# Optimization experiments

Hardware: AMD Instinct MI355X
Metric: run time of the kernel (lower is better)

The kernel has to match this reference:

```python
import jax, jax.numpy as jnp
import numpy as np
import math

N = 4096      # nodes
E = 131072    # edges
D = 256       # hidden / out_features
DIN = 16      # distance_map feature dim
H = 2         # attention heads
HD = D // H   # head dim = 128


def setup_inputs() -> dict:
    key = jax.random.key(0)
    ks = jax.random.split(key, 20)
    s = 0.02
    return {
        "input": jax.random.normal(ks[0], (N, D), jnp.float32),
        "adj": jax.random.randint(ks[1], (2, E), 0, N, jnp.int64),
        "h0": jax.random.normal(ks[2], (N, D), jnp.float32),
        "lamda": 1,
        "alpha": jax.random.uniform(ks[3], (1,), jnp.float32),
        "l": 1,
        "distance_map": jax.random.normal(ks[4], (E, DIN), jnp.float32),
        "norm": jax.random.uniform(ks[5], (E,), jnp.float32),
        # GraphConvolution params
        "weight_local": jax.random.normal(ks[6], (2 * D, D), jnp.float32) * s,
        "weight_global": jax.random.normal(ks[7], (2 * D, D), jnp.float32) * s,
        # EA_GCN.lin : Linear(16, D)
        "lin_w": jax.random.normal(ks[8], (D, DIN), jnp.float32) * s,
        "lin_b": jnp.zeros((D,), jnp.float32),
        # EA_GCN.W_EV : 3D -> 2D -> D -> 16 (GELU between)
        "w1": jax.random.normal(ks[9], (2 * D, 3 * D), jnp.float32) * s,
        "b1": jnp.zeros((2 * D,), jnp.float32),
        "w2": jax.random.normal(ks[10], (D, 2 * D), jnp.float32) * s,
        "b2": jnp.zeros((D,), jnp.float32),
        "w3": jax.random.normal(ks[11], (DIN, D), jnp.float32) * s,
        "b3": jnp.zeros((DIN,), jnp.float32),
        # MultiheadAttention params (torch layout: in_proj [3D, D])
        "in_proj_w": jax.random.normal(ks[12], (3 * D, D), jnp.float32) * s,
        "in_proj_b": jnp.zeros((3 * D,), jnp.float32),
        "out_proj_w": jax.random.normal(ks[13], (D, D), jnp.float32) * s,
        "out_proj_b": jnp.zeros((D,), jnp.float32),
    }


def _mha(x, wi, bi, wo, bo):
    # torch MHA, unbatched (N, D) input, eval mode (dropout off)
    qkv = x @ wi.T + bi                      # [N, 3D]
    q, k, v = jnp.split(qkv, 3, axis=-1)
    q = q.reshape(N, H, HD).transpose(1, 0, 2)  # [H, N, HD]
    k = k.reshape(N, H, HD).transpose(1, 0, 2)
    v = v.reshape(N, H, HD).transpose(1, 0, 2)
    scores = jnp.einsum("hnd,hmd->hnm", q, k) / math.sqrt(HD)
    attn = jax.nn.softmax(scores, axis=-1)
    o = jnp.einsum("hnm,hmd->hnd", attn, v)     # [H, N, HD]
    o = o.transpose(1, 0, 2).reshape(N, D)
    return o @ wo.T + bo


def _ea_gcn(x, edge_index, norm, distance_map, lin_w, lin_b, w1, b1, w2, b2, w3, b3):
    src, dst = edge_index[0], edge_index[1]
    edge_attr = distance_map @ lin_w.T + lin_b               # [E, D]
    msg = norm[:, None] * (x[src] + edge_attr)               # gather + combine
    agg = jax.ops.segment_sum(msg, dst, num_segments=N)      # scatter-add
    x_out = agg + x
    h = jnp.concatenate([x_out[src], edge_attr, x_out[dst]], axis=-1)  # [E, 3D]
    h = jax.nn.gelu(h @ w1.T + b1, approximate=False)
    h = jax.nn.gelu(h @ w2.T + b2, approximate=False)
    dm_out = h @ w3.T + b3                                   # [E, 16]
    return x_out, dm_out


def reference(input, adj, h0, lamda, alpha, l, distance_map, norm,
              weight_local, weight_global, lin_w, lin_b,
              w1, b1, w2, b2, w3, b3,
              in_proj_w, in_proj_b, out_proj_w, out_proj_b):
    theta = min(1.0, math.log(lamda / l + 1.0))
    a = alpha[0]
    h_local, dm_out = _ea_gcn(input, adj, norm, distance_map,
                              lin_w, lin_b, w1, b1, w2, b2, w3, b3)
    h_global = _mha(input, in_proj_w, in_proj_b, out_proj_w, out_proj_b)
    support_local = jnp.concatenate([h_local, h0], axis=1)   # [N, 2D]
    r_local = (1.0 - a) * h_local + a * h0
    support_global = jnp.concatenate([h_global, h0], axis=1)
    r_global = (1.0 - a) * h_global + a * h0
    output_local = theta * (support_local @ weight_local) + (1.0 - theta) * r_local
    output_global = theta * (support_global @ weight_global) + (1.0 - theta) * r_global
    output = output_local + output_global                    # residual=False
    return (output, dm_out)
```

## Files before the change

### kernel.cpp

```cpp
#include <hip/hip_runtime.h>
#include <hip/hip_bf16.h>
#include <math.h>

constexpr int N_   = 4096;
constexpr int E_   = 131072;
constexpr int D_   = 256;
constexpr int DIN_ = 16;
constexpr int D3_  = 768;
constexpr int HD_  = 128;

typedef __bf16 bf16_8 __attribute__((ext_vector_type(8)));
typedef float  f32x4  __attribute__((ext_vector_type(4)));
typedef float  f32x4v __attribute__((ext_vector_type(4)));
typedef unsigned int u32x4 __attribute__((ext_vector_type(4)));

__device__ __forceinline__ unsigned short f2b(float f) {
  unsigned int u = __float_as_uint(f);
  u = u + 0x7fffu + ((u >> 16) & 1u);
  return (unsigned short)(u >> 16);
}
__device__ __forceinline__ float b2f(unsigned short s) {
  return __uint_as_float(((unsigned int)s) << 16);
}
__device__ __forceinline__ unsigned int pack2(unsigned short lo, unsigned short hi) {
  return (unsigned int)lo | ((unsigned int)hi << 16);
}
__device__ __forceinline__ bf16_8 frag16(const unsigned short* p) {
  uint4 v = *(const uint4*)p;
  return __builtin_bit_cast(bf16_8, v);
}
__device__ __forceinline__ float4 ntload4(const void* p) {
  f32x4v v = __builtin_nontemporal_load((const f32x4v*)p);
  float4 r;
  r.x = v[0]; r.y = v[1]; r.z = v[2]; r.w = v[3];
  return r;
}
__device__ __forceinline__ void ntstore16(void* dst, uint4 v) {
  __builtin_nontemporal_store(__builtin_bit_cast(u32x4, v), (u32x4*)dst);
}
__device__ __forceinline__ void gl2lds16(const unsigned short* g, unsigned short* l) {
  __builtin_amdgcn_global_load_lds(
      (const __attribute__((address_space(1))) void*)g,
      (__attribute__((address_space(3))) void*)l, 16, 0, 0);
}

__device__ __forceinline__ float scalar_as_float(const void* p) {
  int iv = *(const int*)p;
  if (iv >= 1 && iv <= 1000000) return (float)iv;
  return __int_as_float(iv);
}

__device__ __forceinline__ float gelu_exact(float v) {
  return 0.5f * v * (1.0f + erff(v * 0.70710678118654752f));
}
__device__ __forceinline__ float gelu_fast(float v) {
  float u = 0.7978845608028654f * v * (1.0f + 0.044715f * v * v);
  return v / (1.0f + __expf(-2.0f * u));
}

__global__ void k_f2b(const float* __restrict__ src, unsigned short* __restrict__ dst, int n) {
  int i = blockIdx.x * 256 + threadIdx.x;
  if (i < n) dst[i] = f2b(src[i]);
}

__global__ void k_prep_w(const float* __restrict__ w1, const float* __restrict__ w2,
                         const float* __restrict__ w3, const float* __restrict__ lin_w,
                         const float* __restrict__ ipw, const float* __restrict__ opw,
                         unsigned short* __restrict__ wb1, unsigned short* __restrict__ wb2,
                         unsigned short* __restrict__ wb3, unsigned short* __restrict__ lwb,
                         unsigned short* __restrict__ wqb, unsigned short* __restrict__ opwb) {
  int i = blockIdx.x * 256 + threadIdx.x;
  if (i < 393216) { wb1[i] = f2b(w1[i]); return; }
  i -= 393216;
  if (i < 131072) { wb2[i] = f2b(w2[i]); return; }
  i -= 131072;
  if (i < 4096) { wb3[i] = f2b(w3[i]); return; }
  i -= 4096;
  if (i < 4096) { lwb[i] = f2b(lin_w[i]); return; }
  i -= 4096;
  if (i < 196608) { wqb[i] = f2b(ipw[i]); return; }
  i -= 196608;
  if (i < 65536) { opwb[i] = f2b(opw[i]); }
}

__global__ void k_prep_t(const float* __restrict__ Wl, const float* __restrict__ Wg,
                         unsigned short* __restrict__ wlT, unsigned short* __restrict__ wgT) {
  int i = blockIdx.x * 256 + threadIdx.x;
  int seg = i >> 17;
  int idx = i & 131071;
  int k = idx & 511, j = idx >> 9;
  const float* src = seg ? Wg : Wl;
  unsigned short* dst = seg ? wgT : wlT;
  dst[idx] = f2b(src[(size_t)k * 256 + j]);
}

__global__ void k_prep_x(const float* __restrict__ input, const float* __restrict__ h0,
                         unsigned short* __restrict__ inb, unsigned short* __restrict__ h0b) {
  int i = blockIdx.x * 256 + threadIdx.x;
  int seg = i >> 20;
  int idx = i & 1048575;
  if (seg) h0b[idx] = f2b(h0[idx]);
  else     inb[idx] = f2b(input[idx]);
}

__global__ void k_copy4(const float4* __restrict__ src, float4* __restrict__ dst, int n4) {
  int idx = blockIdx.x * 256 + threadIdx.x;
  if (idx < n4) dst[idx] = src[idx];
}

__global__ __launch_bounds__(256) void k_edge_attr_mfma(
    const float* __restrict__ dmap, const unsigned short* __restrict__ lwb,
    const float* __restrict__ lin_b, unsigned short* __restrict__ eab) {
  __shared__ unsigned short sT[4][16][264];
  const int tid  = threadIdx.x;
  const int lane = tid & 63, wv = tid >> 6;
  const int r16  = lane & 15, quad = lane >> 4;
  const int e0   = blockIdx.x * 64 + wv * 16;

  const uint4 z4 = make_uint4(0u, 0u, 0u, 0u);
  bf16_8 bfr[16];
#pragma unroll
  for (int n = 0; n < 16; ++n) {
    uint4 v = z4;
    if (quad < 2) v = *(const uint4*)(lwb + (size_t)(n * 16 + r16) * DIN_ + quad * 8);
    bfr[n] = __builtin_bit_cast(bf16_8, v);
  }
  bf16_8 af;
  {
    uint4 p = z4;
    if (quad < 2) {
      const float4* dp = (const float4*)(dmap + (size_t)(e0 + r16) * DIN_ + quad * 8);
      float4 a = dp[0], b = dp[1];
      p = make_uint4(pack2(f2b(a.x), f2b(a.y)), pack2(f2b(a.z), f2b(a.w)),
                     pack2(f2b(b.x), f2b(b.y)), pack2(f2b(b.z), f2b(b.w)));
    }
    af = __builtin_bit_cast(bf16_8, p);
  }

  const f32x4 zz = {0.f, 0.f, 0.f, 0.f};
  f32x4 acc[16];
#pragma unroll
  for (int n = 0; n < 16; ++n) acc[n] = zz;
#pragma unroll
  for (int n = 0; n < 16; ++n)
    acc[n] = __builtin_amdgcn_mfma_f32_16x16x32_bf16(af, bfr[n], acc[n], 0, 0, 0);

#pragma unroll
  for (int n = 0; n < 16; ++n) {
    float bb = lin_b[n * 16 + r16];
#pragma unroll
    for (int rg = 0; rg < 4; ++rg)
      sT[wv][quad * 4 + rg][n * 16 + r16] = f2b(acc[n][rg] + bb);
  }
#pragma unroll
  for (int it = 0; it < 8; ++it) {
    int flat = it * 64 + lane;
    int row = flat >> 5, g = flat & 31;
    uint4 v = *(const uint4*)&sT[wv][row][g * 8];
    ntstore16(&eab[(size_t)(e0 + row) * D_ + g * 8], v);
  }
}

__global__ void k_zero(int* __restrict__ p, int n) {
  int i = blockIdx.x * 256 + threadIdx.x;
  if (i < n) p[i] = 0;
}
__global__ void k_hist(const int* __restrict__ adj, int* __restrict__ cnt) {
  int e = blockIdx.x * 256 + threadIdx.x;
  atomicAdd(&cnt[adj[E_ + e]], 1);
}
__global__ __launch_bounds__(1024) void k_scan(const int* __restrict__ cnt,
                                               int* __restrict__ off, int* __restrict__ cur) {
  __shared__ int ps[1024];
  int tid = threadIdx.x;
  int base = tid * 4;
  int a0 = cnt[base], a1 = cnt[base + 1], a2 = cnt[base + 2], a3 = cnt[base + 3];
  int tsum = a0 + a1 + a2 + a3;
  ps[tid] = tsum;
  __syncthreads();
  for (int st = 1; st < 1024; st <<= 1) {
    int v = (tid >= st) ? ps[tid - st] : 0;
    __syncthreads();
    ps[tid] += v;
    __syncthreads();
  }
  int excl = ps[tid] - tsum;
  int o0 = excl, o1 = excl + a0, o2 = o1 + a1, o3 = o2 + a2;
  off[base] = o0; off[base + 1] = o1; off[base + 2] = o2; off[base + 3] = o3;
  cur[base] = o0; cur[base + 1] = o1; cur[base + 2] = o2; cur[base + 3] = o3;
  if (tid == 1023) off[4096] = o3 + a3;
}
__global__ void k_bucket(const int* __restrict__ adj, int* __restrict__ cur,
                         int* __restrict__ perm) {
  int e = blockIdx.x * 256 + threadIdx.x;
  int p = atomicAdd(&cur[adj[E_ + e]], 1);
  perm[p] = e;
}
__global__ __launch_bounds__(256) void k_gather(
    const float* __restrict__ x, const int* __restrict__ adj,
    const unsigned short* __restrict__ eab, const float* __restrict__ nrm,
    const int* __restrict__ off, const int* __restrict__ perm,
    float* __restrict__ xout) {
  int n = blockIdx.x, t = threadIdx.x;
  int beg = off[n], end = off[n + 1];
  float acc = x[(size_t)n * D_ + t];
  int i = beg;
  for (; i + 1 < end; i += 2) {
    int e0 = perm[i], e1 = perm[i + 1];
    int s0 = adj[e0], s1 = adj[e1];
    float w0 = nrm[e0], w1 = nrm[e1];
    float xa = x[(size_t)s0 * D_ + t];
    float xb = x[(size_t)s1 * D_ + t];
    float ea0 = b2f(eab[(size_t)e0 * D_ + t]);
    float ea1 = b2f(eab[(size_t)e1 * D_ + t]);
    acc += w0 * (xa + ea0) + w1 * (xb + ea1);
  }
  if (i < end) {
    int e0 = perm[i];
    int s0 = adj[e0];
    float w0 = nrm[e0];
    acc += w0 * (x[(size_t)s0 * D_ + t] + b2f(eab[(size_t)e0 * D_ + t]));
  }
  xout[(size_t)n * D_ + t] = acc;
}

__global__ __launch_bounds__(256) void k_scatter(
    const float* __restrict__ x, const int* __restrict__ adj,
    const float* __restrict__ dmap, const float* __restrict__ nrm,
    const float* __restrict__ lin_w, const float* __restrict__ lin_b,
    float* __restrict__ xout) {
  __shared__ float s_dm[4][DIN_];
  int te = threadIdx.x >> 6;
  int d4 = threadIdx.x & 63;
  int e  = blockIdx.x * 4 + te;
  if (d4 < DIN_) s_dm[te][d4] = dmap[(size_t)e * DIN_ + d4];
  __syncthreads();
  int vs = adj[e];
  int vd = adj[E_ + e];
  float w = nrm[e];
  int d = d4 * 4;
  float4 xs = *(const float4*)(x + (size_t)vs * D_ + d);
  float ea[4];
#pragma unroll
  for (int q = 0; q < 4; q++) {
    const float* lw = lin_w + (size_t)(d + q) * DIN_;
    float acc = lin_b[d + q];
#pragma unroll
    for (int k = 0; k < DIN_; k++) acc += s_dm[te][k] * lw[k];
    ea[q] = acc;
  }
  float* op = xout + (size_t)vd * D_ + d;
  atomicAdd(op + 0, w * (xs.x + ea[0]));
  atomicAdd(op + 1, w * (xs.y + ea[1]));
  atomicAdd(op + 2, w * (xs.z + ea[2]));
  atomicAdd(op + 3, w * (xs.w + ea[3]));
}

__global__ __launch_bounds__(256) void k_gemm_bt(
    const float* __restrict__ A, const float* __restrict__ B,
    const float* __restrict__ bias, float* __restrict__ C,
    int M, int Nn, int K) {
  __shared__ float sA[16][68];
  __shared__ float sB[16][68];
  int bm = blockIdx.y * 64, bn = blockIdx.x * 64;
  int tid = threadIdx.x;
  int tr = tid >> 4, tc = tid & 15;
  float acc[4][4] = {};
  for (int k0 = 0; k0 < K; k0 += 16) {
    for (int i = tid; i < 1024; i += 256) {
      int r = i >> 4, c = i & 15;
      sA[c][r] = A[(size_t)(bm + r) * K + k0 + c];
      sB[c][r] = B[(size_t)(bn + r) * K + k0 + c];
    }
    __syncthreads();
#pragma unroll
    for (int kk = 0; kk < 16; kk++) {
      float av[4], bv[4];
#pragma unroll
      for (int i = 0; i < 4; i++) av[i] = sA[kk][tr * 4 + i];
#pragma unroll
      for (int j = 0; j < 4; j++) bv[j] = sB[kk][tc * 4 + j];
#pragma unroll
      for (int i = 0; i < 4; i++)
#pragma unroll
        for (int j = 0; j < 4; j++) acc[i][j] += av[i] * bv[j];
    }
    __syncthreads();
  }
#pragma unroll
  for (int i = 0; i < 4; i++) {
    int r = bm + tr * 4 + i;
#pragma unroll
    for (int j = 0; j < 4; j++) {
      int c = bn + tc * 4 + j;
      C[(size_t)r * Nn + c] = acc[i][j] + bias[c];
    }
  }
}

__global__ __launch_bounds__(256) void k_qkv_mfma(
    const unsigned short* __restrict__ inb, const unsigned short* __restrict__ wqb,
    const float* __restrict__ ipb, float* __restrict__ qkv) {
  __shared__ unsigned short sA[128][72];
  __shared__ unsigned short sB[128][72];
  const int b   = blockIdx.x;
  const int j0  = (b % 6) * 128;
  const int m0  = (b / 6) * 128;
  const int tid = threadIdx.x;
  const int lane = tid & 63, wv = tid >> 6;
  const int r16  = lane & 15, quad = lane >> 4;
  const int sr   = tid >> 1, sh = (tid & 1) * 32;

  const unsigned short* ra = inb + (size_t)(m0 + sr) * D_;
  const unsigned short* rb = wqb + (size_t)(j0 + sr) * D_;

  const f32x4 zz = {0.f, 0.f, 0.f, 0.f};
  f32x4 acc[2][8];
#pragma unroll
  for (int m = 0; m < 2; ++m)
#pragma unroll
    for (int n = 0; n < 8; ++n) acc[m][n] = zz;

  for (int ki = 0; ki < 4; ++ki) {
    __syncthreads();
    {
      const uint4* s    = (const uint4*)(ra + ki * 64 + sh);
      const uint4* bsrc = (const uint4*)(rb + ki * 64 + sh);
      uint4* da = (uint4*)&sA[sr][sh];
      uint4* db = (uint4*)&sB[sr][sh];
#pragma unroll
      for (int i = 0; i < 4; ++i) { da[i] = s[i]; db[i] = bsrc[i]; }
    }
    __syncthreads();
#pragma unroll
    for (int kk = 0; kk < 2; ++kk) {
      bf16_8 a0 = frag16(&sA[wv * 32 + r16][kk * 32 + quad * 8]);
      bf16_8 a1 = frag16(&sA[wv * 32 + 16 + r16][kk * 32 + quad * 8]);
#pragma unroll
      for (int n = 0; n < 8; ++n) {
        bf16_8 bf = frag16(&sB[n * 16 + r16][kk * 32 + quad * 8]);
        acc[0][n] = __builtin_amdgcn_mfma_f32_16x16x32_bf16(a0, bf, acc[0][n], 0, 0, 0);
        acc[1][n] = __builtin_amdgcn_mfma_f32_16x16x32_bf16(a1, bf, acc[1][n], 0, 0, 0);
      }
    }
  }
#pragma unroll
  for (int m = 0; m < 2; ++m)
#pragma unroll
    for (int n = 0; n < 8; ++n) {
      int col = j0 + n * 16 + r16;
      float bb = ipb[col];
#pragma unroll
      for (int rg = 0; rg < 4; ++rg) {
        int row = m0 + wv * 32 + m * 16 + quad * 4 + rg;
        qkv[(size_t)row * D3_ + col] = acc[m][n][rg] + bb;
      }
    }
}

__global__ __launch_bounds__(256) void k_node_pac(
    const unsigned short* __restrict__ xbp, const unsigned short* __restrict__ wb1,
    unsigned short* __restrict__ Pac) {
  __shared__ unsigned short sA[128][72];
  __shared__ unsigned short sB[128][72];
  const int b    = blockIdx.x;
  const int j0   = (b & 7) * 128;
  const int m0   = (b >> 3) * 128;
  const int side = j0 >> 9;
  const int jr   = j0 - side * 512;
  const int tid  = threadIdx.x;
  const int lane = tid & 63, wv = tid >> 6;
  const int r16  = lane & 15, quad = lane >> 4;
  const int sr   = tid >> 1, sh = (tid & 1) * 32;

  const unsigned short* ra = xbp + (size_t)(m0 + sr) * D_;
  const unsigned short* rb = wb1 + (size_t)(jr + sr) * 768 + side * 512;
// ... 242 lines not shown
  const int lane = tid & 63;
  const int wv   = tid >> 6;
  const int r16  = lane & 15;
  const int quad = lane >> 4;

  bf16_8 qf[4];
#pragma unroll
  for (int kk = 0; kk < 4; ++kk)
    qf[kk] = frag16(Qb + (size_t)h * N_ * HD_ + (size_t)(q0 + r16) * HD_ + kk * 32 + quad * 8);

  if (tid < 16) { sm[tid] = -1e30f; sl[tid] = 0.f; }

  const f32x4 zz = {0.f, 0.f, 0.f, 0.f};
  f32x4 o0 = zz, o1 = zz;

  const unsigned short* Kh = Kb + (size_t)h * N_ * HD_;
  const unsigned short* Vh = Vt + (size_t)h * HD_ * N_;

  for (int c0 = 0; c0 < N_; c0 += 64) {
    __syncthreads();
#pragma unroll
    for (int it = 0; it < 4; ++it) {
      int off = (tid + it * 256) * 8;
      int key = off >> 7, d = off & 127;
      *(uint4*)&sK[key][d] = *(const uint4*)(Kh + (size_t)(c0 + key) * HD_ + d);
    }
#pragma unroll
    for (int it = 0; it < 4; ++it) {
      int off = (tid + it * 256) * 8;
      int d = off >> 6, k = off & 63;
      *(uint4*)&sV[d][k] = *(const uint4*)(Vh + (size_t)d * N_ + c0 + k);
    }
    __syncthreads();
    f32x4 s = zz;
#pragma unroll
    for (int kk = 0; kk < 4; ++kk) {
      bf16_8 bf = frag16(&sK[wv * 16 + r16][kk * 32 + quad * 8]);
      s = __builtin_amdgcn_mfma_f32_16x16x32_bf16(qf[kk], bf, s, 0, 0, 0);
    }
    const float sc = 0.08838834764831845f;
#pragma unroll
    for (int r = 0; r < 4; ++r)
      sS[quad * 4 + r][wv * 16 + r16] = s[r] * sc;
    __syncthreads();
    {
      int row = tid >> 4, i = tid & 15;
      float4 v = *(const float4*)&sS[row][i * 4];
      float mx = fmaxf(fmaxf(v.x, v.y), fmaxf(v.z, v.w));
#pragma unroll
      for (int m = 1; m <= 8; m <<= 1) mx = fmaxf(mx, __shfl_xor(mx, m));
      float mo = sm[row];
      float mn = fmaxf(mo, mx);
      float p0 = __expf(v.x - mn), p1 = __expf(v.y - mn);
      float p2 = __expf(v.z - mn), p3 = __expf(v.w - mn);
      float ps = p0 + p1 + p2 + p3;
#pragma unroll
      for (int m = 1; m <= 8; m <<= 1) ps += __shfl_xor(ps, m);
      uint2 pk = {pack2(f2b(p0), f2b(p1)), pack2(f2b(p2), f2b(p3))};
      *(uint2*)&sP[row][i * 4] = pk;
      if (i == 0) {
        float al = __expf(mo - mn);
        sl[row] = sl[row] * al + ps;
        sm[row] = mn;
        sa[row] = al;
      }
    }
    __syncthreads();
    {
      float al0 = sa[quad * 4 + 0], al1 = sa[quad * 4 + 1];
      float al2 = sa[quad * 4 + 2], al3 = sa[quad * 4 + 3];
      o0[0] *= al0; o0[1] *= al1; o0[2] *= al2; o0[3] *= al3;
      o1[0] *= al0; o1[1] *= al1; o1[2] *= al2; o1[3] *= al3;
#pragma unroll
      for (int kk = 0; kk < 2; ++kk) {
        bf16_8 pa = frag16(&sP[r16][kk * 32 + quad * 8]);
        bf16_8 v0 = frag16(&sV[wv * 32 + r16][kk * 32 + quad * 8]);
        bf16_8 v1 = frag16(&sV[wv * 32 + 16 + r16][kk * 32 + quad * 8]);
        o0 = __builtin_amdgcn_mfma_f32_16x16x32_bf16(pa, v0, o0, 0, 0, 0);
        o1 = __builtin_amdgcn_mfma_f32_16x16x32_bf16(pa, v1, o1, 0, 0, 0);
      }
    }
  }
  {
    float i0 = 1.f / sl[quad * 4 + 0], i1 = 1.f / sl[quad * 4 + 1];
    float i2 = 1.f / sl[quad * 4 + 2], i3 = 1.f / sl[quad * 4 + 3];
    float vv[8];
    vv[0] = o0[0] * i0; vv[1] = o0[1] * i1; vv[2] = o0[2] * i2; vv[3] = o0[3] * i3;
    vv[4] = o1[0] * i0; vv[5] = o1[1] * i1; vv[6] = o1[2] * i2; vv[7] = o1[3] * i3;
#pragma unroll
    for (int g = 0; g < 2; ++g)
#pragma unroll
      for (int rg = 0; rg < 4; ++rg) {
        size_t idx = (size_t)(q0 + quad * 4 + rg) * D_ + h * HD_ + wv * 32 + g * 16 + r16;
        float v = vv[g * 4 + rg];
        o_out[idx] = v;
        ob[idx] = f2b(v);
      }
  }
}

__global__ __launch_bounds__(256) void k_final(
    const float* __restrict__ hl, const float* __restrict__ hg, const float* __restrict__ h0,
    const float* __restrict__ Wl, const float* __restrict__ Wg,
    const float* __restrict__ alpha_p, const void* lamda_p, const void* l_p,
    float* __restrict__ out) {
  __shared__ float sA[16][68];
  __shared__ float sB[16][68];
  float theta = fminf(1.f, logf(scalar_as_float(lamda_p) / scalar_as_float(l_p) + 1.f));
  float a = alpha_p[0];
  int bm = blockIdx.y * 64, bn = blockIdx.x * 64;
  int tid = threadIdx.x, tr = tid >> 4, tc = tid & 15;
  float acc[4][4] = {};
  for (int k0 = 0; k0 < 1024; k0 += 16) {
    for (int i = tid; i < 1024; i += 256) {
      int r = i >> 4, c = i & 15;
      int k = k0 + c;
      const float* src = (k < 256) ? hl : (k < 512) ? h0 : (k < 768) ? hg : h0;
      sA[c][r] = src[(size_t)(bm + r) * 256 + (k & 255)];
    }
    for (int i = tid; i < 1024; i += 256) {
      int kk = i >> 6, j = i & 63;
      int k = k0 + kk;
      const float* Bp = (k < 512) ? (Wl + (size_t)k * 256) : (Wg + (size_t)(k - 512) * 256);
      sB[kk][j] = Bp[bn + j];
    }
    __syncthreads();
#pragma unroll
    for (int kk = 0; kk < 16; kk++) {
      float av[4], bv[4];
#pragma unroll
      for (int i = 0; i < 4; i++) av[i] = sA[kk][tr * 4 + i];
#pragma unroll
      for (int j = 0; j < 4; j++) bv[j] = sB[kk][tc * 4 + j];
#pragma unroll
      for (int i = 0; i < 4; i++)
#pragma unroll
        for (int j = 0; j < 4; j++) acc[i][j] += av[i] * bv[j];
    }
    __syncthreads();
  }
  float omt = 1.f - theta;
#pragma unroll
  for (int i = 0; i < 4; i++) {
    int r = bm + tr * 4 + i;
#pragma unroll
    for (int j = 0; j < 4; j++) {
      int c = bn + tc * 4 + j;
      size_t idx = (size_t)r * 256 + c;
      out[idx] = theta * acc[i][j] + omt * ((1.f - a) * (hl[idx] + hg[idx]) + 2.f * a * h0[idx]);
    }
  }
}

__global__ __launch_bounds__(256, 4) void k_mlp_gemm1b(
    const unsigned short* __restrict__ eab, const int* __restrict__ adj,
    const unsigned short* __restrict__ Pac, const unsigned short* __restrict__ wb1,
    const float* __restrict__ b1, unsigned short* __restrict__ t1) {
  __shared__ unsigned short shm[16384];
  unsigned short* lA = shm;
  unsigned short* lB = shm + 8192;
  const int b    = blockIdx.x;
  const int c0   = (b >> 10) * 128;
  const int e0   = (b & 1023) * 128;
  const int tid  = threadIdx.x;
  const int lane = tid & 63, wv = tid >> 6;
  const int r16  = lane & 15, quad = lane >> 4;

  const int row0 = e0 + wv * 32 + r16;
  const int row1 = row0 + 16;
  const unsigned short* ea0 = eab + (size_t)row0 * D_ + quad * 8;
  const unsigned short* ea1 = eab + (size_t)row1 * D_ + quad * 8;

  const f32x4 zz = {0.f, 0.f, 0.f, 0.f};
  f32x4 acc[2][8];
#pragma unroll
  for (int m = 0; m < 2; ++m)
#pragma unroll
    for (int n = 0; n < 8; ++n) acc[m][n] = zz;

  for (int ki = 0; ki < 4; ++ki) {
    __syncthreads();
    {
#pragma unroll
      for (int kk = 0; kk < 2; ++kk) {
        gl2lds16(ea0 + ki * 64 + kk * 32, &lA[(wv * 4 + kk) * 512]);
        gl2lds16(ea1 + ki * 64 + kk * 32, &lA[(wv * 4 + 2 + kk) * 512]);
#pragma unroll
        for (int i = 0; i < 2; ++i) {
          int n = wv * 2 + i;
          gl2lds16(wb1 + (size_t)(c0 + n * 16 + r16) * 768 + 256 + ki * 64 + kk * 32 + quad * 8,
                   &lB[(n * 2 + kk) * 512]);
        }
      }
    }
    __builtin_amdgcn_s_waitcnt(0);
    __syncthreads();
#pragma unroll
    for (int kk = 0; kk < 2; ++kk) {
      bf16_8 a0 = frag16(&lA[(wv * 4 + kk) * 512 + lane * 8]);
      bf16_8 a1 = frag16(&lA[(wv * 4 + 2 + kk) * 512 + lane * 8]);
#pragma unroll
      for (int n = 0; n < 8; ++n) {
        bf16_8 bf = frag16(&lB[(n * 2 + kk) * 512 + lane * 8]);
        acc[0][n] = __builtin_amdgcn_mfma_f32_16x16x32_bf16(a0, bf, acc[0][n], 0, 0, 0);
        acc[1][n] = __builtin_amdgcn_mfma_f32_16x16x32_bf16(a1, bf, acc[1][n], 0, 0, 0);
      }
    }
  }
  __syncthreads();
  unsigned short* reg = shm + wv * 2176;
#pragma unroll
  for (int m = 0; m < 2; ++m) {
#pragma unroll
    for (int n = 0; n < 8; ++n)
#pragma unroll
      for (int rg = 0; rg < 4; ++rg)
        reg[(quad * 4 + rg) * 136 + n * 16 + r16] = f2b(acc[m][n][rg]);
#pragma unroll
    for (int it = 0; it < 4; ++it) {
      int flat = it * 64 + lane;
      int row = flat >> 4;
      int g   = flat & 15;
      int er  = e0 + wv * 32 + m * 16 + row;
      int vs  = adj[er];
      int vd  = adj[E_ + er];
      int c   = c0 + g * 8;
      uint4 midq = *(const uint4*)&reg[row * 136 + g * 8];
      uint4 paq  = *(const uint4*)(Pac + (size_t)vs * 1024 + c);
      uint4 pcq  = *(const uint4*)(Pac + (size_t)vd * 1024 + 512 + c);
      float4 ba = *(const float4*)(b1 + c);
      float4 bb = *(const float4*)(b1 + c + 4);
      const unsigned int mv[4] = {midq.x, midq.y, midq.z, midq.w};
      const unsigned int pv[4] = {paq.x, paq.y, paq.z, paq.w};
      const unsigned int cv[4] = {pcq.x, pcq.y, pcq.z, pcq.w};
      const float bl[8] = {ba.x, ba.y, ba.z, ba.w, bb.x, bb.y, bb.z, bb.w};
      unsigned short us[8];
#pragma unroll
      for (int j = 0; j < 8; ++j) {
        unsigned short mw = (j & 1) ? (unsigned short)(mv[j >> 1] >> 16)
                                    : (unsigned short)(mv[j >> 1] & 0xffffu);
        unsigned short pw = (j & 1) ? (unsigned short)(pv[j >> 1] >> 16)
                                    : (unsigned short)(pv[j >> 1] & 0xffffu);
        unsigned short cw = (j & 1) ? (unsigned short)(cv[j >> 1] >> 16)
                                    : (unsigned short)(cv[j >> 1] & 0xffffu);
        float v = b2f(mw) + b2f(pw) + b2f(cw) + bl[j];
        us[j] = f2b(gelu_fast(v));
      }
      uint4 ov = make_uint4(pack2(us[0], us[1]), pack2(us[2], us[3]),
                            pack2(us[4], us[5]), pack2(us[6], us[7]));
      ntstore16(&t1[(size_t)er * 512 + c], ov);
    }
  }
}

__global__ __launch_bounds__(256, 2) void k_mlp_gemm23(
    const unsigned short* __restrict__ t1, const unsigned short* __restrict__ wb2,
    const float* __restrict__ b2, const unsigned short* __restrict__ wb3,
    const float* __restrict__ b3, float* __restrict__ dmo) {
  __shared__ unsigned short shm[24576];
  unsigned short* lA = shm;
  unsigned short* lB = shm + 8192;
  const int e0   = blockIdx.x * 128;
  const int tid  = threadIdx.x;
  const int lane = tid & 63, wv = tid >> 6;
  const int r16  = lane & 15, quad = lane >> 4;

  const int row0 = e0 + wv * 32 + r16;
  const int row1 = row0 + 16;
  const unsigned short* pa0 = t1 + (size_t)row0 * 512 + quad * 8;
  const unsigned short* pa1 = t1 + (size_t)row1 * 512 + quad * 8;

  const f32x4 zz = {0.f, 0.f, 0.f, 0.f};
  f32x4 acc[2][16];
#pragma unroll
  for (int m = 0; m < 2; ++m)
#pragma unroll
    for (int n = 0; n < 16; ++n) acc[m][n] = zz;

  for (int ki = 0; ki < 8; ++ki) {
    __syncthreads();
    {
#pragma unroll
      for (int kk = 0; kk < 2; ++kk) {
        gl2lds16(pa0 + ki * 64 + kk * 32, &lA[(wv * 4 + kk) * 512]);
        gl2lds16(pa1 + ki * 64 + kk * 32, &lA[(wv * 4 + 2 + kk) * 512]);
#pragma unroll
        for (int i = 0; i < 4; ++i) {
          int n = wv * 4 + i;
          gl2lds16(wb2 + (size_t)(n * 16 + r16) * 512 + ki * 64 + kk * 32 + quad * 8,
                   &lB[(n * 2 + kk) * 512]);
        }
      }
    }
    __builtin_amdgcn_s_waitcnt(0);
    __syncthreads();
#pragma unroll
    for (int kk = 0; kk < 2; ++kk) {
      bf16_8 a0 = frag16(&lA[(wv * 4 + kk) * 512 + lane * 8]);
      bf16_8 a1 = frag16(&lA[(wv * 4 + 2 + kk) * 512 + lane * 8]);
#pragma unroll
      for (int n = 0; n < 16; ++n) {
        bf16_8 bf = frag16(&lB[(n * 2 + kk) * 512 + lane * 8]);
        acc[0][n] = __builtin_amdgcn_mfma_f32_16x16x32_bf16(a0, bf, acc[0][n], 0, 0, 0);
        acc[1][n] = __builtin_amdgcn_mfma_f32_16x16x32_bf16(a1, bf, acc[1][n], 0, 0, 0);
      }
    }
  }
  __syncthreads();
  unsigned short* reg = shm + wv * 4224;
  float bb3 = b3[r16];
#pragma unroll
  for (int m = 0; m < 2; ++m) {
#pragma unroll
    for (int n = 0; n < 16; ++n) {
      float bb = b2[n * 16 + r16];
#pragma unroll
      for (int rg = 0; rg < 4; ++rg)
        reg[(quad * 4 + rg) * 264 + n * 16 + r16] = f2b(gelu_fast(acc[m][n][rg] + bb));
    }
    f32x4 acc3 = zz;
#pragma unroll
    for (int ks = 0; ks < 8; ++ks) {
      bf16_8 a = frag16(&reg[r16 * 264 + ks * 32 + quad * 8]);
      bf16_8 b = frag16(wb3 + (size_t)r16 * 256 + ks * 32 + quad * 8);
      acc3 = __builtin_amdgcn_mfma_f32_16x16x32_bf16(a, b, acc3, 0, 0, 0);
    }
#pragma unroll
    for (int rg = 0; rg < 4; ++rg)
      dmo[(size_t)(e0 + wv * 32 + m * 16 + quad * 4 + rg) * DIN_ + r16] = acc3[rg] + bb3;
  }
}

__global__ __launch_bounds__(256, 3) void k_edge_mlp_mfma(
    const float* __restrict__ xout, const int* __restrict__ adj,
    const float* __restrict__ dmap,
    const float* __restrict__ lin_w, const float* __restrict__ lin_b,
    const unsigned short* __restrict__ wb1, const float* __restrict__ b1,
    const unsigned short* __restrict__ wb2, const float* __restrict__ b2,
    const unsigned short* __restrict__ wb3, const float* __restrict__ b3,
    float* __restrict__ dmo) {
  __shared__ unsigned short sLo[8448];
  __shared__ unsigned short sT1[32][520];
  unsigned short (*sA)[136]  = (unsigned short(*)[136])sLo;
  unsigned short (*sT2)[264] = (unsigned short(*)[264])sLo;

  const int tid  = threadIdx.x;
  const int e0   = blockIdx.x * 32;
  const int lane = tid & 63;
  const int wv   = tid >> 6;
  const int r16  = lane & 15;
  const int quad = lane >> 4;

  const int sr = tid >> 3;
  const int t8 = tid & 7;
  const int se = e0 + sr;
  const int vsrc = adj[se];
  const int vdst = adj[E_ + se];

  float4 pf0, pf1, pf2, pf3;
  float4 dm0, dm1, dm2, dm3;
  {
    const float4* sp = (const float4*)(xout + (size_t)vsrc * D_ + t8 * 16);
    pf0 = sp[0]; pf1 = sp[1]; pf2 = sp[2]; pf3 = sp[3];
  }

  const f32x4 zz = {0.f, 0.f, 0.f, 0.f};
  f32x4 acc1[8][2];
#pragma unroll
  for (int i = 0; i < 8; ++i) { acc1[i][0] = zz; acc1[i][1] = zz; }

  for (int c = 0; c < 6; ++c) {
    const int k0 = c * 128;
    __syncthreads();
    {
      unsigned short tmp[16];
      if (c == 2 || c == 3) {
        int jb = (c - 2) * 128 + t8 * 16;
#pragma unroll
        for (int j = 0; j < 16; ++j) {
          const float4* lw = (const float4*)(lin_w + (size_t)(jb + j) * DIN_);
          float4 w0 = lw[0], w1 = lw[1], w2 = lw[2], w3 = lw[3];
          float acc = lin_b[jb + j];
          acc += dm0.x * w0.x + dm0.y * w0.y + dm0.z * w0.z + dm0.w * w0.w;
          acc += dm1.x * w1.x + dm1.y * w1.y + dm1.z * w1.z + dm1.w * w1.w;
          acc += dm2.x * w2.x + dm2.y * w2.y + dm2.z * w2.z + dm2.w * w2.w;
          acc += dm3.x * w3.x + dm3.y * w3.y + dm3.z * w3.z + dm3.w * w3.w;
          tmp[j] = f2b(acc);
        }
      } else {
        tmp[0]  = f2b(pf0.x); tmp[1]  = f2b(pf0.y); tmp[2]  = f2b(pf0.z); tmp[3]  = f2b(pf0.w);
        tmp[4]  = f2b(pf1.x); tmp[5]  = f2b(pf1.y); tmp[6]  = f2b(pf1.z); tmp[7]  = f2b(pf1.w);
        tmp[8]  = f2b(pf2.x); tmp[9]  = f2b(pf2.y); tmp[10] = f2b(pf2.z); tmp[11] = f2b(pf2.w);
        tmp[12] = f2b(pf3.x); tmp[13] = f2b(pf3.y); tmp[14] = f2b(pf3.z); tmp[15] = f2b(pf3.w);
      }
      unsigned short* dstp = &sA[sr][t8 * 16];
      uint4 q0v = {pack2(tmp[0], tmp[1]),   pack2(tmp[2], tmp[3]),
                   pack2(tmp[4], tmp[5]),   pack2(tmp[6], tmp[7])};
      uint4 q1v = {pack2(tmp[8], tmp[9]),   pack2(tmp[10], tmp[11]),
                   pack2(tmp[12], tmp[13]), pack2(tmp[14], tmp[15])};
      *(uint4*)(dstp) = q0v;
      *(uint4*)(dstp + 8) = q1v;
    }
    if (c == 0) {
      const float4* sp = (const float4*)(xout + (size_t)vsrc * D_ + 128 + t8 * 16);
      pf0 = sp[0]; pf1 = sp[1]; pf2 = sp[2]; pf3 = sp[3];
    } else if (c == 1) {
      const float4* dp = (const float4*)(dmap + (size_t)se * DIN_);
      dm0 = ntload4(dp); dm1 = ntload4(dp + 1); dm2 = ntload4(dp + 2); dm3 = ntload4(dp + 3);
    } else if (c == 3) {
      const float4* sp = (const float4*)(xout + (size_t)vdst * D_ + t8 * 16);
      pf0 = sp[0]; pf1 = sp[1]; pf2 = sp[2]; pf3 = sp[3];
    } else if (c == 4) {
      const float4* sp = (const float4*)(xout + (size_t)vdst * D_ + 128 + t8 * 16);
      pf0 = sp[0]; pf1 = sp[1]; pf2 = sp[2]; pf3 = sp[3];
    }
    __syncthreads();
#pragma unroll
    for (int kk = 0; kk < 4; ++kk) {
      bf16_8 a0 = frag16(&sA[r16][kk * 32 + quad * 8]);
      bf16_8 a1 = frag16(&sA[16 + r16][kk * 32 + quad * 8]);
#pragma unroll
      for (int i = 0; i < 8; ++i) {
        const unsigned short* bp =
            wb1 + (size_t)(wv * 128 + i * 16 + r16) * 768 + k0 + kk * 32 + quad * 8;
        bf16_8 bf = frag16(bp);
        acc1[i][0] = __builtin_amdgcn_mfma_f32_16x16x32_bf16(a0, bf, acc1[i][0], 0, 0, 0);
        acc1[i][1] = __builtin_amdgcn_mfma_f32_16x16x32_bf16(a1, bf, acc1[i][1], 0, 0, 0);
      }
    }
  }
#pragma unroll
  for (int i = 0; i < 8; ++i) {
    int col = wv * 128 + i * 16 + r16;
    float bb = b1[col];
#pragma unroll
    for (int r = 0; r < 4; ++r) {
      int row = quad * 4 + r;
      sT1[row][col] = f2b(gelu_exact(acc1[i][0][r] + bb));
      sT1[row + 16][col] = f2b(gelu_exact(acc1[i][1][r] + bb));
    }
  }
  __syncthreads();

  f32x4 acc2[4][2];
#pragma unroll
  for (int i = 0; i < 4; ++i) { acc2[i][0] = zz; acc2[i][1] = zz; }
#pragma unroll 4
  for (int ks = 0; ks < 16; ++ks) {
    bf16_8 a0 = frag16(&sT1[r16][ks * 32 + quad * 8]);
    bf16_8 a1 = frag16(&sT1[16 + r16][ks * 32 + quad * 8]);
#pragma unroll
    for (int i = 0; i < 4; ++i) {
      const unsigned short* bp =
          wb2 + (size_t)(wv * 64 + i * 16 + r16) * 512 + ks * 32 + quad * 8;
      bf16_8 bf = frag16(bp);
      acc2[i][0] = __builtin_amdgcn_mfma_f32_16x16x32_bf16(a0, bf, acc2[i][0], 0, 0, 0);
      acc2[i][1] = __builtin_amdgcn_mfma_f32_16x16x32_bf16(a1, bf, acc2[i][1], 0, 0, 0);
    }
  }
#pragma unroll
  for (int i = 0; i < 4; ++i) {
    int col = wv * 64 + i * 16 + r16;
    float bb = b2[col];
#pragma unroll
    for (int m = 0; m < 2; ++m)
#pragma unroll
      for (int r = 0; r < 4; ++r) {
        int row = m * 16 + quad * 4 + r;
        sT2[row][col] = f2b(gelu_exact(acc2[i][m][r] + bb));
      }
  }
  __syncthreads();

  if (wv < 2) {
    f32x4 acc3 = zz;
#pragma unroll
    for (int ks = 0; ks < 8; ++ks) {
      bf16_8 a = frag16(&sT2[wv * 16 + r16][ks * 32 + quad * 8]);
      bf16_8 b = frag16(wb3 + (size_t)r16 * 256 + ks * 32 + quad * 8);
      acc3 = __builtin_amdgcn_mfma_f32_16x16x32_bf16(a, b, acc3, 0, 0, 0);
    }
    float bb = b3[r16];
#pragma unroll
    for (int r = 0; r < 4; ++r) {
      int row = wv * 16 + quad * 4 + r;
      __builtin_nontemporal_store(acc3[r] + bb, &dmo[(size_t)(e0 + row) * DIN_ + r16]);
    }
  }
}

extern "C" void kernel_launch(void* const* d_in, const int* in_sizes, int n_in,
                              void* d_out, int out_size, void* d_ws, size_t ws_size,
                              hipStream_t stream) {
  const float* input = (const float*)d_in[0];
  const int*   adj   = (const int*)d_in[1];
  const float* h0    = (const float*)d_in[2];
  const void*  lamda = d_in[3];
  const float* alpha = (const float*)d_in[4];
  const void*  lll   = d_in[5];
  const float* dmap  = (const float*)d_in[6];
  const float* nrm   = (const float*)d_in[7];
  const float* Wl    = (const float*)d_in[8];
  const float* Wg    = (const float*)d_in[9];
  const float* lin_w = (const float*)d_in[10];
  const float* lin_b = (const float*)d_in[11];
  const float* w1    = (const float*)d_in[12];
  const float* b1    = (const float*)d_in[13];
  const float* w2    = (const float*)d_in[14];
  const float* b2    = (const float*)d_in[15];
  const float* w3    = (const float*)d_in[16];
  const float* b3    = (const float*)d_in[17];
  const float* ipw   = (const float*)d_in[18];
  const float* ipb   = (const float*)d_in[19];
  const float* opw   = (const float*)d_in[20];
  const float* opb   = (const float*)d_in[21];
  float* out = (float*)d_out;
  float* dmo = out + (size_t)N_ * D_;

  float* ws   = (float*)d_ws;
  float* xout = ws;
  float* qkv  = xout + (size_t)N_ * D_;
  float* atto = qkv  + (size_t)N_ * 3 * D_;
  float* hgl  = atto + (size_t)N_ * D_;
  unsigned short* wb1 = (unsigned short*)(hgl + (size_t)N_ * D_);
  unsigned short* wb2 = wb1 + 512 * 768;
  unsigned short* wb3 = wb2 + 256 * 512;
  unsigned short* Qb  = wb3 + 16 * 256;
  unsigned short* Kb  = Qb + 2 * N_ * HD_;
  unsigned short* Vt  = Kb + 2 * N_ * HD_;
  unsigned short* t1b = Vt + 2 * HD_ * N_;
  unsigned short* t2b = t1b + (size_t)E_ * 512;
  unsigned short* eab = t2b;
  int* cnt  = (int*)(t2b + (size_t)E_ * 256);
  int* off  = cnt + 4096;
  int* cur  = off + 4100;
  int* perm = cur + 4096;
  unsigned short* xbp = (unsigned short*)(perm + E_);
  unsigned short* lwb = xbp + (size_t)N_ * D_;
  unsigned short* inb = lwb + 256 * DIN_;
  unsigned short* h0b = inb + (size_t)N_ * D_;
  unsigned short* hgb = h0b + (size_t)N_ * D_;
  unsigned short* wqb = hgb + (size_t)N_ * D_;
  unsigned short* wlT = wqb + 768 * 256;
  unsigned short* wgT = wlT + 256 * 512;
  unsigned short* opwb = wgT + 256 * 512;
  unsigned short* attob = (unsigned short*)qkv;
  unsigned short* Pac = (unsigned short*)qkv;
  const size_t fast_need = (size_t)((char*)(opwb + 256 * 256) - (char*)d_ws);
  const bool fast = ws_size >= fast_need;

  if (fast) {
    k_prep_w<<<dim3((794624 + 255) / 256), 256, 0, stream>>>(
        w1, w2, w3, lin_w, ipw, opw, wb1, wb2, wb3, lwb, wqb, opwb);
    k_prep_t<<<dim3((262144 + 255) / 256), 256, 0, stream>>>(Wl, Wg, wlT, wgT);
    k_prep_x<<<dim3((2097152 + 255) / 256), 256, 0, stream>>>(input, h0, inb, h0b);

    k_edge_attr_mfma<<<dim3(E_ / 64), 256, 0, stream>>>(dmap, lwb, lin_b, eab);
    k_zero<<<dim3(16), 256, 0, stream>>>(cnt, 4096);
    k_hist<<<dim3(E_ / 256), 256, 0, stream>>>(adj, cnt);
    k_scan<<<dim3(1), 1024, 0, stream>>>(cnt, off, cur);
    k_bucket<<<dim3(E_ / 256), 256, 0, stream>>>(adj, cur, perm);
    k_gather<<<dim3(N_), 256, 0, stream>>>(input, adj, eab, nrm, off, perm, xout);
    k_f2b<<<dim3(N_ * D_ / 256), 256, 0, stream>>>(xout, xbp, N_ * D_);

    k_qkv_mfma<<<dim3(192), 256, 0, stream>>>(inb, wqb, ipb, qkv);
    k_qk2b<<<dim3(N_ * 512 / 8 / 256), 256, 0, stream>>>(qkv, Qb, Kb);
    k_v2t<<<dim3(N_ / 64, 2), 256, 0, stream>>>(qkv, Vt);
    k_attn_mfma<<<dim3(N_ / 16, 2), 256, 0, stream>>>(Qb, Kb, Vt, atto, attob);
    k_outproj_mfma<<<dim3(64), 256, 0, stream>>>(attob, opwb, opb, hgl, hgb);

    k_final_mfma<<<dim3(64), 256, 0, stream>>>(xbp, h0b, hgb, wlT, wgT,
                                               xout, hgl, h0, alpha, lamda, lll, out);

    k_node_pac<<<dim3(256), 256, 0, stream>>>(xbp, wb1, Pac);
    k_mlp_gemm1b<<<dim3(E_ / 128 * 4), 256, 0, stream>>>(eab, adj, Pac, wb1, b1, t1b);
    k_mlp_gemm23<<<dim3(E_ / 128), 256, 0, stream>>>(t1b, wb2, b2, wb3, b3, dmo);
  } else {
    k_f2b<<<dim3((512 * 768 + 255) / 256), 256, 0, stream>>>(w1, wb1, 512 * 768);
    k_f2b<<<dim3((256 * 512 + 255) / 256), 256, 0, stream>>>(w2, wb2, 256 * 512);
    k_f2b<<<dim3((16 * 256 + 255) / 256), 256, 0, stream>>>(w3, wb3, 16 * 256);
    k_copy4<<<dim3(N_ * D_ / 4 / 256), 256, 0, stream>>>((const float4*)input, (float4*)xout,
                                                         N_ * D_ / 4);
    k_scatter<<<dim3(E_ / 4), 256, 0, stream>>>(input, adj, dmap, nrm, lin_w, lin_b, xout);
    k_gemm_bt<<<dim3(D3_ / 64, N_ / 64), 256, 0, stream>>>(input, ipw, ipb, qkv, N_, D3_, D_);
    k_qk2b<<<dim3(N_ * 512 / 8 / 256), 256, 0, stream>>>(qkv, Qb, Kb);
    k_v2t<<<dim3(N_ / 64, 2), 256, 0, stream>>>(qkv, Vt);
    k_attn_mfma<<<dim3(N_ / 16, 2), 256, 0, stream>>>(Qb, Kb, Vt, atto, (unsigned short*)qkv);
    k_gemm_bt<<<dim3(D_ / 64, N_ / 64), 256, 0, stream>>>(atto, opw, opb, hgl, N_, D_, D_);
    k_final<<<dim3(4, N_ / 64), 256, 0, stream>>>(xout, hgl, h0, Wl, Wg, alpha, lamda, lll, out);
    k_edge_mlp_mfma<<<dim3(E_ / 32), 256, 0, stream>>>(xout, adj, dmap, lin_w, lin_b,
                                                       wb1, b1, wb2, b2, wb3, b3, dmo);
  }
}
```

Measured before the change: 582.4 us.

## Fold edge-attr linear into W1 and gather, drop materialized edge attributes

```diff
diff --git a/kernel.cpp b/kernel.cpp
--- a/kernel.cpp
+++ b/kernel.cpp
@@ -83,6 +83,23 @@
   if (i < 65536) { opwb[i] = f2b(opw[i]); }
 }
 
+__global__ __launch_bounds__(256) void k_prep_m(
+    const float* __restrict__ w1, const float* __restrict__ lin_w,
+    const float* __restrict__ lin_b, const float* __restrict__ b1,
+    unsigned short* __restrict__ Mb, float* __restrict__ cbv) {
+  int idx = blockIdx.x * 256 + threadIdx.x;
+  int j = idx >> 4, i = idx & 15;
+  const float* wr = w1 + (size_t)j * 768 + 256;
+  float acc = 0.f;
+  for (int kk = 0; kk < 256; ++kk) acc += wr[kk] * lin_w[kk * 16 + i];
+  Mb[j * 16 + i] = f2b(acc);
+  if (i == 0) {
+    float c = b1[j];
+    for (int kk = 0; kk < 256; ++kk) c += wr[kk] * lin_b[kk];
+    cbv[j] = c;
+  }
+}
+
 __global__ void k_prep_t(const float* __restrict__ Wl, const float* __restrict__ Wg,
                          unsigned short* __restrict__ wlT, unsigned short* __restrict__ wgT) {
   int i = blockIdx.x * 256 + threadIdx.x;
@@ -106,59 +123,6 @@
 __global__ void k_copy4(const float4* __restrict__ src, float4* __restrict__ dst, int n4) {
   int idx = blockIdx.x * 256 + threadIdx.x;
   if (idx < n4) dst[idx] = src[idx];
-}
-
-__global__ __launch_bounds__(256) void k_edge_attr_mfma(
-    const float* __restrict__ dmap, const unsigned short* __restrict__ lwb,
-    const float* __restrict__ lin_b, unsigned short* __restrict__ eab) {
-  __shared__ unsigned short sT[4][16][264];
-  const int tid  = threadIdx.x;
-  const int lane = tid & 63, wv = tid >> 6;
-  const int r16  = lane & 15, quad = lane >> 4;
-  const int e0   = blockIdx.x * 64 + wv * 16;
-
-  const uint4 z4 = make_uint4(0u, 0u, 0u, 0u);
-  bf16_8 bfr[16];
-#pragma unroll
-  for (int n = 0; n < 16; ++n) {
-    uint4 v = z4;
-    if (quad < 2) v = *(const uint4*)(lwb + (size_t)(n * 16 + r16) * DIN_ + quad * 8);
-    bfr[n] = __builtin_bit_cast(bf16_8, v);
-  }
-  bf16_8 af;
-  {
-    uint4 p = z4;
-    if (quad < 2) {
-      const float4* dp = (const float4*)(dmap + (size_t)(e0 + r16) * DIN_ + quad * 8);
-      float4 a = dp[0], b = dp[1];
-      p = make_uint4(pack2(f2b(a.x), f2b(a.y)), pack2(f2b(a.z), f2b(a.w)),
-                     pack2(f2b(b.x), f2b(b.y)), pack2(f2b(b.z), f2b(b.w)));
-    }
-    af = __builtin_bit_cast(bf16_8, p);
-  }
-
-  const f32x4 zz = {0.f, 0.f, 0.f, 0.f};
-  f32x4 acc[16];
-#pragma unroll
-  for (int n = 0; n < 16; ++n) acc[n] = zz;
-#pragma unroll
-  for (int n = 0; n < 16; ++n)
-    acc[n] = __builtin_amdgcn_mfma_f32_16x16x32_bf16(af, bfr[n], acc[n], 0, 0, 0);
-
-#pragma unroll
-  for (int n = 0; n < 16; ++n) {
-    float bb = lin_b[n * 16 + r16];
-#pragma unroll
-    for (int rg = 0; rg < 4; ++rg)
-      sT[wv][quad * 4 + rg][n * 16 + r16] = f2b(acc[n][rg] + bb);
-  }
-#pragma unroll
-  for (int it = 0; it < 8; ++it) {
-    int flat = it * 64 + lane;
-    int row = flat >> 5, g = flat & 31;
-    uint4 v = *(const uint4*)&sT[wv][row][g * 8];
-    ntstore16(&eab[(size_t)(e0 + row) * D_ + g * 8], v);
-  }
 }
 
 __global__ void k_zero(int* __restrict__ p, int n) {
@@ -198,30 +162,46 @@
 }
 __global__ __launch_bounds__(256) void k_gather(
     const float* __restrict__ x, const int* __restrict__ adj,
-    const unsigned short* __restrict__ eab, const float* __restrict__ nrm,
+    const float* __restrict__ dmap, const float* __restrict__ nrm,
+    const float* __restrict__ lin_w, const float* __restrict__ lin_b,
     const int* __restrict__ off, const int* __restrict__ perm,
     float* __restrict__ xout) {
+  __shared__ float sds[17];
   int n = blockIdx.x, t = threadIdx.x;
   int beg = off[n], end = off[n + 1];
   float acc = x[(size_t)n * D_ + t];
+  float ds = 0.f, ws = 0.f;
   int i = beg;
   for (; i + 1 < end; i += 2) {
     int e0 = perm[i], e1 = perm[i + 1];
     int s0 = adj[e0], s1 = adj[e1];
     float w0 = nrm[e0], w1 = nrm[e1];
-    float xa = x[(size_t)s0 * D_ + t];
-    float xb = x[(size_t)s1 * D_ + t];
-    float ea0 = b2f(eab[(size_t)e0 * D_ + t]);
-    float ea1 = b2f(eab[(size_t)e1 * D_ + t]);
-    acc += w0 * (xa + ea0) + w1 * (xb + ea1);
+    acc += w0 * x[(size_t)s0 * D_ + t] + w1 * x[(size_t)s1 * D_ + t];
+    if (t < DIN_) {
+      ds += w0 * dmap[(size_t)e0 * DIN_ + t] + w1 * dmap[(size_t)e1 * DIN_ + t];
+      ws += w0 + w1;
+    }
   }
   if (i < end) {
     int e0 = perm[i];
     int s0 = adj[e0];
     float w0 = nrm[e0];
-    acc += w0 * (x[(size_t)s0 * D_ + t] + b2f(eab[(size_t)e0 * D_ + t]));
-  }
-  xout[(size_t)n * D_ + t] = acc;
+    acc += w0 * x[(size_t)s0 * D_ + t];
+    if (t < DIN_) {
+      ds += w0 * dmap[(size_t)e0 * DIN_ + t];
+      ws += w0;
+    }
+  }
+  if (t < DIN_) { sds[t] = ds; if (t == 0) sds[16] = ws; }
+  __syncthreads();
+  float ex = sds[16] * lin_b[t];
+  const float4* lw = (const float4*)(lin_w + (size_t)t * DIN_);
+  float4 l0 = lw[0], l1 = lw[1], l2 = lw[2], l3 = lw[3];
+  ex += sds[0] * l0.x + sds[1] * l0.y + sds[2] * l0.z + sds[3] * l0.w;
+  ex += sds[4] * l1.x + sds[5] * l1.y + sds[6] * l1.z + sds[7] * l1.w;
+  ex += sds[8] * l2.x + sds[9] * l2.y + sds[10] * l2.z + sds[11] * l2.w;
+  ex += sds[12] * l3.x + sds[13] * l3.y + sds[14] * l3.z + sds[15] * l3.w;
+  xout[(size_t)n * D_ + t] = acc + ex;
 }
 
 __global__ __launch_bounds__(256) void k_scatter(
@@ -770,13 +750,11 @@
   }
 }
 
-__global__ __launch_bounds__(256, 4) void k_mlp_gemm1b(
-    const unsigned short* __restrict__ eab, const int* __restrict__ adj,
-    const unsigned short* __restrict__ Pac, const unsigned short* __restrict__ wb1,
-    const float* __restrict__ b1, unsigned short* __restrict__ t1) {
-  __shared__ unsigned short shm[16384];
-  unsigned short* lA = shm;
-  unsigned short* lB = shm + 8192;
+__global__ __launch_bounds__(256, 4) void k_mlp_gemm1c(
+    const float* __restrict__ dmap, const int* __restrict__ adj,
+    const unsigned short* __restrict__ Pac, const unsigned short* __restrict__ Mb,
+    const float* __restrict__ cbv, unsigned short* __restrict__ t1) {
+  __shared__ unsigned short shm[8704];
   const int b    = blockIdx.x;
   const int c0   = (b >> 10) * 128;
   const int e0   = (b & 1023) * 128;
@@ -784,48 +762,33 @@
   const int lane = tid & 63, wv = tid >> 6;
   const int r16  = lane & 15, quad = lane >> 4;
 
-  const int row0 = e0 + wv * 32 + r16;
-  const int row1 = row0 + 16;
-  const unsigned short* ea0 = eab + (size_t)row0 * D_ + quad * 8;
-  const unsigned short* ea1 = eab + (size_t)row1 * D_ + quad * 8;
+  const uint4 z4 = make_uint4(0u, 0u, 0u, 0u);
+  bf16_8 af[2];
+#pragma unroll
+  for (int m = 0; m < 2; ++m) {
+    uint4 p = z4;
+    if (quad < 2) {
+      const int edge = e0 + wv * 32 + m * 16 + r16;
+      const float4* dp = (const float4*)(dmap + (size_t)edge * DIN_ + quad * 8);
+      float4 a = dp[0], bq = dp[1];
+      p = make_uint4(pack2(f2b(a.x), f2b(a.y)), pack2(f2b(a.z), f2b(a.w)),
+                     pack2(f2b(bq.x), f2b(bq.y)), pack2(f2b(bq.z), f2b(bq.w)));
+    }
+    af[m] = __builtin_bit_cast(bf16_8, p);
+  }
 
   const f32x4 zz = {0.f, 0.f, 0.f, 0.f};
   f32x4 acc[2][8];
 #pragma unroll
-  for (int m = 0; m < 2; ++m)
-#pragma unroll
-    for (int n = 0; n < 8; ++n) acc[m][n] = zz;
-
-  for (int ki = 0; ki < 4; ++ki) {
-    __syncthreads();
-    {
-#pragma unroll
-      for (int kk = 0; kk < 2; ++kk) {
-        gl2lds16(ea0 + ki * 64 + kk * 32, &lA[(wv * 4 + kk) * 512]);
-        gl2lds16(ea1 + ki * 64 + kk * 32, &lA[(wv * 4 + 2 + kk) * 512]);
-#pragma unroll
-        for (int i = 0; i < 2; ++i) {
-          int n = wv * 2 + i;
-          gl2lds16(wb1 + (size_t)(c0 + n * 16 + r16) * 768 + 256 + ki * 64 + kk * 32 + quad * 8,
-                   &lB[(n * 2 + kk) * 512]);
-        }
-      }
-    }
-    __builtin_amdgcn_s_waitcnt(0);
-    __syncthreads();
-#pragma unroll
-    for (int kk = 0; kk < 2; ++kk) {
-      bf16_8 a0 = frag16(&lA[(wv * 4 + kk) * 512 + lane * 8]);
-      bf16_8 a1 = frag16(&lA[(wv * 4 + 2 + kk) * 512 + lane * 8]);
-#pragma unroll
-      for (int n = 0; n < 8; ++n) {
-        bf16_8 bf = frag16(&lB[(n * 2 + kk) * 512 + lane * 8]);
-        acc[0][n] = __builtin_amdgcn_mfma_f32_16x16x32_bf16(a0, bf, acc[0][n], 0, 0, 0);
-        acc[1][n] = __builtin_amdgcn_mfma_f32_16x16x32_bf16(a1, bf, acc[1][n], 0, 0, 0);
-      }
-    }
-  }
-  __syncthreads();
+  for (int n = 0; n < 8; ++n) {
+    uint4 mv = z4;
+    if (quad < 2)
+      mv = *(const uint4*)(Mb + (size_t)(c0 + n * 16 + r16) * DIN_ + quad * 8);
+    bf16_8 bf = __builtin_bit_cast(bf16_8, mv);
+    acc[0][n] = __builtin_amdgcn_mfma_f32_16x16x32_bf16(af[0], bf, zz, 0, 0, 0);
+    acc[1][n] = __builtin_amdgcn_mfma_f32_16x16x32_bf16(af[1], bf, zz, 0, 0, 0);
+  }
+
   unsigned short* reg = shm + wv * 2176;
 #pragma unroll
   for (int m = 0; m < 2; ++m) {
@@ -846,8 +809,8 @@
       uint4 midq = *(const uint4*)&reg[row * 136 + g * 8];
       uint4 paq  = *(const uint4*)(Pac + (size_t)vs * 1024 + c);
       uint4 pcq  = *(const uint4*)(Pac + (size_t)vd * 1024 + 512 + c);
-      float4 ba = *(const float4*)(b1 + c);
-      float4 bb = *(const float4*)(b1 + c + 4);
+      float4 ba = *(const float4*)(cbv + c);
+      float4 bb = *(const float4*)(cbv + c + 4);
       const unsigned int mv[4] = {midq.x, midq.y, midq.z, midq.w};
       const unsigned int pv[4] = {paq.x, paq.y, paq.z, paq.w};
       const unsigned int cv[4] = {pcq.x, pcq.y, pcq.z, pcq.w};
@@ -1148,7 +1111,6 @@
   unsigned short* Vt  = Kb + 2 * N_ * HD_;
   unsigned short* t1b = Vt + 2 * HD_ * N_;
   unsigned short* t2b = t1b + (size_t)E_ * 512;
-  unsigned short* eab = t2b;
   int* cnt  = (int*)(t2b + (size_t)E_ * 256);
   int* off  = cnt + 4096;
   int* cur  = off + 4100;
@@ -1164,6 +1126,8 @@
   unsigned short* opwb = wgT + 256 * 512;
   unsigned short* attob = (unsigned short*)qkv;
   unsigned short* Pac = (unsigned short*)qkv;
+  unsigned short* Mb_ = t2b;
+  float* cbv = (float*)(t2b + 8192);
   const size_t fast_need = (size_t)((char*)(opwb + 256 * 256) - (char*)d_ws);
   const bool fast = ws_size >= fast_need;
 
@@ -1172,13 +1136,14 @@
         w1, w2, w3, lin_w, ipw, opw, wb1, wb2, wb3, lwb, wqb, opwb);
     k_prep_t<<<dim3((262144 + 255) / 256), 256, 0, stream>>>(Wl, Wg, wlT, wgT);
     k_prep_x<<<dim3((2097152 + 255) / 256), 256, 0, stream>>>(input, h0, inb, h0b);
-
-    k_edge_attr_mfma<<<dim3(E_ / 64), 256, 0, stream>>>(dmap, lwb, lin_b, eab);
+    k_prep_m<<<dim3(32), 256, 0, stream>>>(w1, lin_w, lin_b, b1, Mb_, cbv);
+
     k_zero<<<dim3(16), 256, 0, stream>>>(cnt, 4096);
     k_hist<<<dim3(E_ / 256), 256, 0, stream>>>(adj, cnt);
     k_scan<<<dim3(1), 1024, 0, stream>>>(cnt, off, cur);
     k_bucket<<<dim3(E_ / 256), 256, 0, stream>>>(adj, cur, perm);
-    k_gather<<<dim3(N_), 256, 0, stream>>>(input, adj, eab, nrm, off, perm, xout);
+    k_gather<<<dim3(N_), 256, 0, stream>>>(input, adj, dmap, nrm, lin_w, lin_b,
+                                           off, perm, xout);
     k_f2b<<<dim3(N_ * D_ / 256), 256, 0, stream>>>(xout, xbp, N_ * D_);
 
     k_qkv_mfma<<<dim3(192), 256, 0, stream>>>(inb, wqb, ipb, qkv);
@@ -1191,7 +1156,7 @@
                                                xout, hgl, h0, alpha, lamda, lll, out);
 
     k_node_pac<<<dim3(256), 256, 0, stream>>>(xbp, wb1, Pac);
-    k_mlp_gemm1b<<<dim3(E_ / 128 * 4), 256, 0, stream>>>(eab, adj, Pac, wb1, b1, t1b);
+    k_mlp_gemm1c<<<dim3(E_ / 128 * 4), 256, 0, stream>>>(dmap, adj, Pac, Mb_, cbv, t1b);
     k_mlp_gemm23<<<dim3(E_ / 128), 256, 0, stream>>>(t1b, wb2, b2, wb3, b3, dmo);
   } else {
     k_f2b<<<dim3((512 * 768 + 255) / 256), 256, 0, stream>>>(w1, wb1, 512 * 768);
```

After: 528.8 us (median of 2 runs). 1.1x faster.
